# Optimization experiments

Measured on AMD Instinct MI355X. Metric: run time of the kernel, lower is better.

Reference implementation:

```python
import jax, jax.numpy as jnp
import numpy as np

T = 2048   # timesteps
S = 512    # state_len (MMD buffer length)
D = 128    # latent_dim


def setup_inputs() -> dict:
    key = jax.random.key(0)
    k1, k2 = jax.random.split(key)
    x = jax.random.normal(k1, (1, T, 1, D), dtype=jnp.float32)
    initial_state = jax.random.normal(k2, (S, D), dtype=jnp.float32)
    return {"x": x, "initial_state": initial_state}


def reference(x, initial_state):
    # x: [1, T, 1, D]; initial_state: [S, D]
    latent_dim = x.shape[-1]
    z_seq = x[0, :, 0, :]  # [T, D] -- batch=1 stream, as the TF module assumes

    def step(d, z):
        # d: [S, D] shifting buffer of past latents; z: [D] current latent
        # polynomial kernel: (1 - ||z - d_i||^2 / latent_dim)^3 for each buffer row
        gamma = (-1.0 / latent_dim) * jnp.sum((z[None, :] - d) ** 2, axis=-1)  # [S]
        poly = (1.0 + gamma) ** 3                                              # [S]
        # shift buffer: newest latent in front, drop oldest
        d_new = jnp.concatenate([z[None, :], d[:-1]], axis=0)                  # [S, D]
        return d_new, poly

    _, kernel = jax.lax.scan(step, initial_state, z_seq)  # kernel: [T, S]
    return kernel[None, :, :]  # [1, T, S] == K.rnn outputs with batch=1
```

## Files before the change

### kernel.cpp

```cpp
#include <hip/hip_runtime.h>

#define T_LEN 2048
#define S_LEN 512
#define D_LEN 128
#define BT 64
#define BG 80
#define THREADS 512


__global__ __launch_bounds__(THREADS, 2)
void mmd_kernel(const float* __restrict__ x, const float* __restrict__ init,
                float* __restrict__ out) {
    __shared__ float lds[(BT + BG) * D_LEN];
    __shared__ float znorm[BT];
    __shared__ float gnorm[BG];

    float* zt = lds;
    float* gt = lds + BT * D_LEN;

    const int bt = blockIdx.y;
    const int j  = blockIdx.x;
    const int t0 = bt * BT;
    const int g0 = t0 + j * BG;

    const int tid = threadIdx.x;

    #pragma unroll
    for (int k = 0; k < 4; ++k) {
        const int idx = tid + k * THREADS;
        const int row = idx >> 5;
        const int c4  = idx & 31;
        const float4 v = *(const float4*)(x + (t0 + row) * D_LEN + c4 * 4);
        *(float4*)(zt + row * D_LEN + ((c4 ^ (row & 7)) << 2)) = v;
        float s = v.x * v.x + v.y * v.y + v.z * v.z + v.w * v.w;
        s += __shfl_xor(s, 1);
        s += __shfl_xor(s, 2);
        s += __shfl_xor(s, 4);
        s += __shfl_xor(s, 8);
        s += __shfl_xor(s, 16);
        if (c4 == 0) znorm[row] = s;
    }
    #pragma unroll
    for (int k = 0; k < 5; ++k) {
        const int idx = tid + k * THREADS;
        const int row = idx >> 5;
        const int c4  = idx & 31;
        int g = g0 + row;
        if (g > T_LEN + S_LEN - 1) g = T_LEN + S_LEN - 1;
        const float* src = (g >= S_LEN) ? (x + (g - S_LEN) * D_LEN)
                                        : (init + (S_LEN - 1 - g) * D_LEN);
        const float4 v = *(const float4*)(src + c4 * 4);
        *(float4*)(gt + row * D_LEN + ((c4 ^ (row & 7)) << 2)) = v;
        float s = v.x * v.x + v.y * v.y + v.z * v.z + v.w * v.w;
        s += __shfl_xor(s, 1);
        s += __shfl_xor(s, 2);
        s += __shfl_xor(s, 4);
        s += __shfl_xor(s, 8);
        s += __shfl_xor(s, 16);
        if (c4 == 0) gnorm[row] = s;
    }
    __syncthreads();

    const int sl = tid >> 8;
    const int id = tid & 255;
    const int tx = id & 15;
    const int ty = id >> 4;

    float dot[4][5];
    #pragma unroll
    for (int i = 0; i < 4; ++i)
        #pragma unroll
        for (int jj = 0; jj < 5; ++jj) dot[i][jj] = 0.f;

    const int zsw = ty & 7;
    const int gsw = tx & 7;
    int zb[4], wb[5];
    #pragma unroll
    for (int i = 0; i < 4; ++i)
        zb[i] = (((2 * sl + i) & 3) * 16 + ty) * D_LEN + sl * 64;
    #pragma unroll
    for (int jj = 0; jj < 5; ++jj)
        wb[jj] = (jj * 16 + tx) * D_LEN + sl * 64;

    #pragma unroll 4
    for (int kk = 0; kk < 16; ++kk) {
        const int zc = (kk ^ zsw) << 2;
        const int gc = (kk ^ gsw) << 2;
        float4 za[4], w[5];
        #pragma unroll
        for (int i = 0; i < 4; ++i)
            za[i] = *(const float4*)(zt + zb[i] + zc);
        #pragma unroll
        for (int jj = 0; jj < 5; ++jj)
            w[jj] = *(const float4*)(gt + wb[jj] + gc);
        #pragma unroll
        for (int i = 0; i < 4; ++i)
            #pragma unroll
            for (int jj = 0; jj < 5; ++jj)
                dot[i][jj] += za[i].x * w[jj].x + za[i].y * w[jj].y
                            + za[i].z * w[jj].z + za[i].w * w[jj].w;
    }
    __syncthreads();

    #pragma unroll
    for (int i = 2; i < 4; ++i) {
        const int gi = (2 * sl + i) & 3;
        #pragma unroll
        for (int jj = 0; jj < 5; ++jj)
            lds[(gi * 5 + jj) * 256 + id] = dot[i][jj];
    }
    __syncthreads();

    #pragma unroll
    for (int i = 0; i < 2; ++i) {
        const int gi = 2 * sl + i;
        const int tr = gi * 16 + ty;
        const int t  = t0 + tr;
        const float zn = znorm[tr];
        #pragma unroll
        for (int jj = 0; jj < 5; ++jj) {
            const float tot = dot[i][jj] + lds[(gi * 5 + jj) * 256 + id];
            const int gr = jj * 16 + tx;
            const int g  = g0 + gr;
            const int so = t + (S_LEN - 1) - g;
            if (so >= 0 && so < S_LEN) {
                const float dist = zn + gnorm[gr] - 2.f * tot;
                const float p = 1.f - dist * (1.f / (float)D_LEN);
                out[t * S_LEN + so] = p * p * p;
            }
        }
    }
}

extern "C" void kernel_launch(void* const* d_in, const int* in_sizes, int n_in,
                              void* d_out, int out_size, void* d_ws, size_t ws_size,
                              hipStream_t stream) {
    (void)in_sizes; (void)n_in; (void)out_size; (void)d_ws; (void)ws_size;
    const float* x    = (const float*)d_in[0];
    const float* init = (const float*)d_in[1];
    float* out = (float*)d_out;

    dim3 grid(8, 32);
    mmd_kernel<<<grid, THREADS, 0, stream>>>(x, init, out);
}
```

Before: 70.45 us.

## Split D-reduction across four thread slices with 8x5 register tiles

Changes the register tiling of the z·g dot-product stage. Threads are now split into four groups of 128, each reducing over a 32-wide slice of D with an 8x5 accumulator tile, where before two groups of 256 each covered a 64-wide slice with a 4x5 tile. Partial sums from the other three slices go through LDS and are combined at the end. This raises per-thread reuse of the g loads and shortens the inner loop. In exchange it needs more accumulator registers, which may push the kernel past its launch bound of 2 blocks, and it adds more LDS traffic for the final reduction.

```diff
diff --git a/kernel.cpp b/kernel.cpp
--- a/kernel.cpp
+++ b/kernel.cpp
@@ -61,66 +61,69 @@
     }
     __syncthreads();
 
-    const int sl = tid >> 8;
-    const int id = tid & 255;
-    const int tx = id & 15;
-    const int ty = id >> 4;
+    const int sl = tid >> 7;
+    const int id = tid & 127;
+    const int px = id & 15;
+    const int py = id >> 4;
 
-    float dot[4][5];
+    float acc[8][5];
     #pragma unroll
-    for (int i = 0; i < 4; ++i)
+    for (int i = 0; i < 8; ++i)
         #pragma unroll
-        for (int jj = 0; jj < 5; ++jj) dot[i][jj] = 0.f;
+        for (int jj = 0; jj < 5; ++jj) acc[i][jj] = 0.f;
 
-    const int zsw = ty & 7;
-    const int gsw = tx & 7;
-    int zb[4], wb[5];
+    const int gsw = px & 7;
+    int zb[8], wb[5];
     #pragma unroll
-    for (int i = 0; i < 4; ++i)
-        zb[i] = (((2 * sl + i) & 3) * 16 + ty) * D_LEN + sl * 64;
+    for (int i = 0; i < 8; ++i)
+        zb[i] = ((((2 * sl + i) & 7) * 8 + py) * D_LEN) + sl * 32;
     #pragma unroll
     for (int jj = 0; jj < 5; ++jj)
-        wb[jj] = (jj * 16 + tx) * D_LEN + sl * 64;
+        wb[jj] = (jj * 16 + px) * D_LEN + sl * 32;
 
-    #pragma unroll 4
-    for (int kk = 0; kk < 16; ++kk) {
-        const int zc = (kk ^ zsw) << 2;
+    #pragma unroll 2
+    for (int kk = 0; kk < 8; ++kk) {
+        const int zc = (kk ^ py) << 2;
         const int gc = (kk ^ gsw) << 2;
-        float4 za[4], w[5];
+        float4 za[8], w[5];
         #pragma unroll
-        for (int i = 0; i < 4; ++i)
+        for (int i = 0; i < 8; ++i)
             za[i] = *(const float4*)(zt + zb[i] + zc);
         #pragma unroll
         for (int jj = 0; jj < 5; ++jj)
             w[jj] = *(const float4*)(gt + wb[jj] + gc);
         #pragma unroll
-        for (int i = 0; i < 4; ++i)
+        for (int i = 0; i < 8; ++i)
             #pragma unroll
             for (int jj = 0; jj < 5; ++jj)
-                dot[i][jj] += za[i].x * w[jj].x + za[i].y * w[jj].y
+                acc[i][jj] += za[i].x * w[jj].x + za[i].y * w[jj].y
                             + za[i].z * w[jj].z + za[i].w * w[jj].w;
     }
     __syncthreads();
 
     #pragma unroll
-    for (int i = 2; i < 4; ++i) {
-        const int gi = (2 * sl + i) & 3;
+    for (int i = 2; i < 8; ++i) {
+        const int gi = (2 * sl + i) & 7;
+        const int src = (i >> 1) - 1;
         #pragma unroll
         for (int jj = 0; jj < 5; ++jj)
-            lds[(gi * 5 + jj) * 256 + id] = dot[i][jj];
+            lds[((gi * 3 + src) * 5 + jj) * 128 + id] = acc[i][jj];
     }
     __syncthreads();
 
     #pragma unroll
     for (int i = 0; i < 2; ++i) {
         const int gi = 2 * sl + i;
-        const int tr = gi * 16 + ty;
+        const int tr = gi * 8 + py;
         const int t  = t0 + tr;
         const float zn = znorm[tr];
         #pragma unroll
         for (int jj = 0; jj < 5; ++jj) {
-            const float tot = dot[i][jj] + lds[(gi * 5 + jj) * 256 + id];
-            const int gr = jj * 16 + tx;
+            float tot = acc[i][jj];
+            #pragma unroll
+            for (int src = 0; src < 3; ++src)
+                tot += lds[((gi * 3 + src) * 5 + jj) * 128 + id];
+            const int gr = jj * 16 + px;
             const int g  = g0 + gr;
             const int so = t + (S_LEN - 1) - g;
             if (so >= 0 && so < S_LEN) {
```

Measured after the change: 68.16 us. 1.03x faster.
